# Kernel optimization log

Measured on AMD Instinct MI355X. Metric: run time of the kernel, lower is better.

The kernel has to match this reference:

```python
import jax, jax.numpy as jnp
import numpy as np

B, C, H, W = 2, 128, 64, 64
EPS = 1e-5


def setup_inputs() -> dict:
    key = jax.random.key(0)
    ks = jax.random.split(key, 8)
    sc = 1.0 / np.sqrt(C)
    inp = {
        "x": jax.random.normal(ks[0], (B, C, H, W, 2), jnp.float32),
        # naive complex BN affine params: per-channel, per-component (real/imag)
        "bn_w": jnp.ones((C, 2), jnp.float32),
        "bn_b": jnp.zeros((C, 2), jnp.float32),
        # complex 1x1 conv weights: (out_c, in_c, 2) -> [..,0]=W_real, [..,1]=W_imag
        "wq": jax.random.normal(ks[1], (C, C, 2), jnp.float32) * sc,
        "bq": jnp.zeros((C, 2), jnp.float32),
        "wk": jax.random.normal(ks[2], (C, C, 2), jnp.float32) * sc,
        "bk": jnp.zeros((C, 2), jnp.float32),
        "wv": jax.random.normal(ks[3], (C, C, 2), jnp.float32) * sc,
        "bv": jnp.zeros((C, 2), jnp.float32),
        "gamma": jnp.float32(0.05),
    }
    return inp


def _complex_bn(x, w, b):
    # naive complex BN: normalize real and imag independently per channel
    # x: (B,C,H,W,2); stats over (B,H,W) per (C, component)
    mean = x.mean(axis=(0, 2, 3), keepdims=True)
    var = x.var(axis=(0, 2, 3), keepdims=True)
    xn = (x - mean) * jax.lax.rsqrt(var + EPS)
    return xn * w[None, :, None, None, :] + b[None, :, None, None, :]


def _complex_conv1x1(x, w, b):
    # x: (B,C,H,W,2); w: (O,C,2); b: (O,2)
    xr, xi = x[..., 0], x[..., 1]
    wr, wi = w[..., 0], w[..., 1]
    yr = jnp.einsum('oc,bchw->bohw', wr, xr) - jnp.einsum('oc,bchw->bohw', wi, xi)
    yi = jnp.einsum('oc,bchw->bohw', wr, xi) + jnp.einsum('oc,bchw->bohw', wi, xr)
    yr = yr + b[:, 0][None, :, None, None]
    yi = yi + b[:, 1][None, :, None, None]
    return jnp.stack([yr, yi], axis=-1)


def _attention(x, wq, bq, wk, bk, wv, bv, gamma):
    scale = C ** (-0.5)
    N = H * W
    # q,k,v: (B,C,H,W,2) -> (B,C,N,2) -> (B,N,C,2)
    to_tokens = lambda t: t.reshape(B, C, N, 2).transpose(0, 2, 1, 3)
    q = to_tokens(_complex_conv1x1(x, wq, bq))
    k = to_tokens(_complex_conv1x1(x, wk, bk))
    v = to_tokens(_complex_conv1x1(x, wv, bv))

    qr, qi = q[..., 0], q[..., 1]          # (B,N,C)
    kr, ki = k[..., 0], -k[..., 1]         # conjugate of k
    # k_t = conj(k) with token/channel axes swapped -> (B,C,N)
    ktr = kr.transpose(0, 2, 1)
    kti = ki.transpose(0, 2, 1)

    # complex matmul q @ k_t -> only the real part is used downstream
    attn_real = jnp.einsum('bnc,bcm->bnm', qr, ktr) - jnp.einsum('bnc,bcm->bnm', qi, kti)
    attn_w = jax.nn.softmax(attn_real * scale, axis=-1)  # (B,N,N)
    # dropout = identity (eval mode)

    # attn is purely real -> complex matmul reduces to two real matmuls
    out_r = jnp.einsum('bnm,bmc->bnc', attn_w, v[..., 0])
    out_i = jnp.einsum('bnm,bmc->bnc', attn_w, v[..., 1])
    out = jnp.stack([out_r, out_i], axis=-1)              # (B,N,C,2)
    out = out.transpose(0, 2, 1, 3).reshape(B, C, H, W, 2)
    return x + gamma * out


def reference(x, bn_w, bn_b, wq, bq, wk, bk, wv, bv, gamma):
    xn = _complex_bn(x, bn_w, bn_b)
    return _attention(xn, wq, bq, wk, bk, wv, bv, gamma)
```

## Files before the change

### kernel.cpp

```cpp
#include <hip/hip_runtime.h>
#include <hip/hip_bf16.h>

typedef __bf16 bf16_t;
typedef __bf16 bf16x8 __attribute__((ext_vector_type(8)));
typedef float  f32x4  __attribute__((ext_vector_type(4)));

#define MFMA16(A,B,C) __builtin_amdgcn_mfma_f32_16x16x32_bf16((A),(B),(C),0,0,0)

constexpr int Bn = 2, Cc = 128, Hh = 64, Wd = 64;
constexpr int N  = Hh * Wd;
constexpr int T  = Bn * N;
constexpr int D  = 2 * Cc;
constexpr int NSP = 4;
constexpr float EPS = 1e-5f;
constexpr float SCL = 0.08838834764831845f * 1.4426950408889634f;

__device__ __forceinline__ int tfrag(int row, int ch) {
    return (((ch >> 5) * 4 + (row >> 4)) << 10) +
           ((((ch >> 3) & 3) * 16 + (row & 15)) << 4) + (ch & 7) * 2;
}
__device__ __forceinline__ int vfrag(int ch, int key) {
    return (((key >> 5) * 16 + (ch >> 4)) << 10) +
           ((((key >> 3) & 3) * 16 + (ch & 15)) << 4) + (key & 7) * 2;
}

__device__ __forceinline__ void gl16(const void* g, void* l) {
    __builtin_amdgcn_global_load_lds(
        (const __attribute__((address_space(1))) void*)g,
        (__attribute__((address_space(3))) void*)l, 16, 0, 0);
}

__global__ void k_pre(const float* __restrict__ x, float4* __restrict__ part,
                      const float* __restrict__ wq, const float* __restrict__ wk,
                      const float* __restrict__ wv, const float* __restrict__ bq,
                      const float* __restrict__ bk, const float* __restrict__ bv,
                      char* __restrict__ Wg, float* __restrict__ bt) {
    int tid = threadIdx.x;
    if (blockIdx.x < 512) {
        int bid = blockIdx.x;
        int q = bid >> 7, c = bid & 127;
        float sr = 0.f, si = 0.f, qr = 0.f, qi = 0.f;
        for (int b = 0; b < Bn; ++b) {
            const float2* p = (const float2*)x + (size_t)(b * Cc + c) * N + q * 1024;
            for (int i = tid; i < 1024; i += 256) {
                float2 v = p[i];
                sr += v.x; si += v.y; qr += v.x * v.x; qi += v.y * v.y;
            }
        }
        #pragma unroll
        for (int d = 32; d >= 1; d >>= 1) {
            sr += __shfl_xor(sr, d); si += __shfl_xor(si, d);
            qr += __shfl_xor(qr, d); qi += __shfl_xor(qi, d);
        }
        __shared__ float red[4][4];
        int w = tid >> 6;
        if ((tid & 63) == 0) { red[w][0] = sr; red[w][1] = si; red[w][2] = qr; red[w][3] = qi; }
        __syncthreads();
        if (tid == 0) {
            part[c * 4 + q] = make_float4(red[0][0] + red[1][0] + red[2][0] + red[3][0],
                                          red[0][1] + red[1][1] + red[2][1] + red[3][1],
                                          red[0][2] + red[1][2] + red[2][2] + red[3][2],
                                          red[0][3] + red[1][3] + red[2][3] + red[3][3]);
        }
    } else {
        int o = blockIdx.x - 512;
        int k = tid;
        int proj = o >> 8, oc = o & 255;
        const float* wsrc = proj == 0 ? wq : (proj == 1 ? wk : wv);
        const float* bsrc = proj == 0 ? bq : (proj == 1 ? bk : bv);
        int co = oc >> 7, oo = oc & 127;
        int c = k & 127, kc = k >> 7;
        float val;
        if (co == 0) val = (kc == 0) ? wsrc[(oo * 128 + c) * 2 + 0] : -wsrc[(oo * 128 + c) * 2 + 1];
        else         val = (kc == 0) ? wsrc[(oo * 128 + c) * 2 + 1] :  wsrc[(oo * 128 + c) * 2 + 0];
        int tile = o >> 6, row = o & 63;
        *(bf16_t*)(Wg + (size_t)tile * 32768 + tfrag(row, k)) = (bf16_t)val;
        if (k == 0) bt[o] = bsrc[oo * 2 + co];
    }
}

__global__ void k_norm(const float* __restrict__ x, const float4* __restrict__ part,
                       const float* __restrict__ bn_w, const float* __restrict__ bn_b,
                       char* __restrict__ XNg) {
    __shared__ float4 ssl[128];
    __shared__ __align__(16) char Tsh[32768];
    int blk = blockIdx.x;
    int b = blk >> 6, hw0 = (blk & 63) * 64;
    int tid = threadIdx.x;
    if (tid < 128) {
        float4 p0 = part[tid * 4 + 0], p1 = part[tid * 4 + 1];
        float4 p2 = part[tid * 4 + 2], p3 = part[tid * 4 + 3];
        float sr = p0.x + p1.x + p2.x + p3.x, si = p0.y + p1.y + p2.y + p3.y;
        float qr = p0.z + p1.z + p2.z + p3.z, qi = p0.w + p1.w + p2.w + p3.w;
        const float inv = 1.0f / (float)(Bn * N);
        float mr = sr * inv, mi = si * inv;
        float vr = qr * inv - mr * mr, vi = qi * inv - mi * mi;
        float scr = bn_w[tid * 2 + 0] * rsqrtf(vr + EPS);
        float sci = bn_w[tid * 2 + 1] * rsqrtf(vi + EPS);
        ssl[tid] = make_float4(scr, bn_b[tid * 2 + 0] - mr * scr,
                               sci, bn_b[tid * 2 + 1] - mi * sci);
    }
    __syncthreads();
    const float2* xin = (const float2*)x;
    #pragma unroll
    for (int it = 0; it < 32; ++it) {
        int idx = it * 256 + tid;
        int c = idx >> 6, hw = idx & 63;
        size_t gi = (size_t)(b * Cc + c) * N + hw0 + hw;
        float2 v = xin[gi];
        float4 s = ssl[c];
        *(bf16_t*)(Tsh + tfrag(hw, c))       = (bf16_t)(v.x * s.x + s.y);
        *(bf16_t*)(Tsh + tfrag(hw, c + 128)) = (bf16_t)(v.y * s.z + s.w);
    }
    __syncthreads();
    #pragma unroll
    for (int it = 0; it < 8; ++it) {
        int idx = it * 256 + tid;
        *(uint4*)(XNg + (size_t)blk * 32768 + idx * 16) = *(const uint4*)(Tsh + idx * 16);
    }
}

__global__ __launch_bounds__(256) void k_qkv(const char* __restrict__ XNg,
        const char* __restrict__ Wg, const float* __restrict__ bt,
        char* __restrict__ Qg, char* __restrict__ Kg, char* __restrict__ Vg) {
    __shared__ __align__(16) char Xsh[32768];
    __shared__ __align__(16) char Wsh[32768];
    int mx = blockIdx.x, ny = blockIdx.y;
    int tid = threadIdx.x;
    int w = tid >> 6, lane = tid & 63, n15 = lane & 15, quad = lane >> 4;
    const char* xs = XNg + (size_t)mx * 32768;
    const char* wsp = Wg + (size_t)ny * 32768;
    #pragma unroll
    for (int i = 0; i < 8; ++i) {
        int off = (w * 8 + i) * 1024 + lane * 16;
        gl16(xs + off, Xsh + off);
        gl16(wsp + off, Wsh + off);
    }
    __syncthreads();
    f32x4 acc[4] = {};
    #pragma unroll
    for (int ks = 0; ks < 8; ++ks) {
        bf16x8 a = *(const bf16x8*)(Xsh + (ks * 4 + w) * 1024 + lane * 16);
        #pragma unroll
        for (int t = 0; t < 4; ++t) {
            bf16x8 bw = *(const bf16x8*)(Wsh + (ks * 4 + t) * 1024 + lane * 16);
            acc[t] = MFMA16(a, bw, acc[t]);
        }
    }
    int proj = ny >> 2;
    int jb = (ny & 3) * 64;
    #pragma unroll
    for (int t = 0; t < 4; ++t) {
        int j = jb + t * 16 + n15;
        float bias = bt[ny * 64 + t * 16 + n15];
        #pragma unroll
        for (int r = 0; r < 4; ++r) {
            int tk = mx * 64 + w * 16 + quad * 4 + r;
            float v = acc[t][r] + bias;
            int bb = tk >> 12, n = tk & (N - 1);
            if (proj == 0) {
                *(bf16_t*)(Qg + (size_t)(tk >> 6) * 32768 + tfrag(tk & 63, j)) = (bf16_t)v;
            } else {
                size_t tb = (size_t)(bb * 64 + (n >> 6)) * 32768;
                if (proj == 1) *(bf16_t*)(Kg + tb + tfrag(n & 63, j)) = (bf16_t)v;
                else           *(bf16_t*)(Vg + tb + vfrag(j, n & 63)) = (bf16_t)v;
            }
        }
    }
}

__global__ __launch_bounds__(256, 2) void k_attn(const char* __restrict__ Qg,
        const char* __restrict__ Kg, const char* __restrict__ Vg,
        bf16_t* __restrict__ Opb, float* __restrict__ Lp) {
    __shared__ __align__(16) char Ksh[2 * 16384];
    __shared__ __align__(16) char Vsh[16384];
    __shared__ __align__(16) char Psh[4096];
    int bid = blockIdx.x;
    int grp = bid & 7, qt = bid >> 3;
    int sp = grp & 3, b = grp >> 2;
    int tid = threadIdx.x;
    int w = tid >> 6, lane = tid & 63, n15 = lane & 15, quad = lane >> 4;
    int r = w >> 1, h = w & 1;

    bf16x8 onef;
    #pragma unroll
    for (int i = 0; i < 8; ++i) onef[i] = (bf16_t)1.0f;

    bf16x8 qf[2][8];
    const char* qb = Qg + (size_t)(b * 64 + qt) * 32768;
    #pragma unroll
    for (int g = 0; g < 2; ++g)
        #pragma unroll
        for (int ks = 0; ks < 8; ++ks)
            qf[g][ks] = *(const bf16x8*)(qb + (ks * 4 + r * 2 + g) * 1024 + lane * 16);

    {
        size_t kt0 = (size_t)(b * 64 + sp * 16) * 32768;
        #pragma unroll
        for (int i = 0; i < 4; ++i) {
            int lf = w * 4 + i;
            gl16(Kg + kt0 + (((lf >> 1) * 4 + (lf & 1)) << 10) + lane * 16,
                 Ksh + (lf << 10) + lane * 16);
        }
    }

    f32x4 o[2][8] = {};
    f32x4 l_[2] = {};

    #pragma unroll 2
    for (int kt = 0; kt < 32; ++kt) {
        int cur = kt & 1;
        __syncthreads();

        size_t vt = (size_t)(b * 64 + sp * 16 + (kt >> 1)) * 32768 +
                    (size_t)(kt & 1) * 16384;
        #pragma unroll
        for (int i = 0; i < 4; ++i) {
            int off = (w * 4 + i) * 1024 + lane * 16;
            gl16(Vg + vt + off, Vsh + off);
        }
        if (kt < 31) {
            int ck = kt + 1;
            size_t ktile = (size_t)(b * 64 + sp * 16 + (ck >> 1)) * 32768;
            char* kb = Ksh + (cur ^ 1) * 16384;
            #pragma unroll
            for (int i = 0; i < 4; ++i) {
                int lf = w * 4 + i;
                gl16(Kg + ktile + (((lf >> 1) * 4 + (ck & 1) * 2 + (lf & 1)) << 10) + lane * 16,
                     kb + (lf << 10) + lane * 16);
            }
        }

        const char* kc = Ksh + cur * 16384;
        f32x4 s0 = {}, s1 = {};
        #pragma unroll
        for (int ks = 0; ks < 8; ++ks) {
            bf16x8 kf = *(const bf16x8*)(kc + ((ks * 2 + h) << 10) + lane * 16);
            s0 = MFMA16(qf[0][ks], kf, s0);
            s1 = MFMA16(qf[1][ks], kf, s1);
        }
        #pragma unroll
        for (int ri = 0; ri < 4; ++ri) {
            float p0 = __builtin_amdgcn_exp2f(s0[ri] * SCL);
            float p1 = __builtin_amdgcn_exp2f(s1[ri] * SCL);
            int base = ((h * 2 + (n15 >> 3)) * 16 + quad * 4 + ri) * 16 + (n15 & 7) * 2;
            *(bf16_t*)(Psh + ((r * 2 + 0) << 10) + base) = (bf16_t)p0;
            *(bf16_t*)(Psh + ((r * 2 + 1) << 10) + base) = (bf16_t)p1;
        }
        if (kt < 31) asm volatile("s_waitcnt vmcnt(4) lgkmcnt(0)" ::: "memory");
        else         asm volatile("s_waitcnt vmcnt(0) lgkmcnt(0)" ::: "memory");
        __builtin_amdgcn_s_barrier();
        __builtin_amdgcn_sched_barrier(0);

        bf16x8 pa0 = *(const bf16x8*)(Psh + ((r * 2 + 0) << 10) + lane * 16);
        bf16x8 pa1 = *(const bf16x8*)(Psh + ((r * 2 + 1) << 10) + lane * 16);
        l_[0] = MFMA16(pa0, onef, l_[0]);
        l_[1] = MFMA16(pa1, onef, l_[1]);
        #pragma unroll
        for (int ct = 0; ct < 8; ++ct) {
            bf16x8 vf = *(const bf16x8*)(Vsh + ((h * 8 + ct) << 10) + lane * 16);
            o[0][ct] = MFMA16(pa0, vf, o[0][ct]);
            o[1][ct] = MFMA16(pa1, vf, o[1][ct]);
        }
    }
    int tok0 = b * N + qt * 64 + r * 32;
    #pragma unroll
    for (int g = 0; g < 2; ++g) {
        #pragma unroll
        for (int ct = 0; ct < 8; ++ct)
            #pragma unroll
            for (int ri = 0; ri < 4; ++ri)
                Opb[((size_t)sp * T + tok0 + g * 16 + quad * 4 + ri) * D +
                    h * 128 + ct * 16 + n15] = (bf16_t)o[g][ct][ri];
        if (h == 0 && n15 == 0) {
            #pragma unroll
            for (int ri = 0; ri < 4; ++ri)
                Lp[sp * T + tok0 + g * 16 + quad * 4 + ri] = l_[g][ri];
        }
    }
}

__global__ void k_comb(const bf16_t* __restrict__ Opb, const float* __restrict__ Lp,
                       const float4* __restrict__ part, const float* __restrict__ bn_w,
                       const float* __restrict__ bn_b, const float* __restrict__ x,
                       const float* __restrict__ gamma, float* __restrict__ out) {
    __shared__ float4 ssl[128];
    __shared__ float wts[32];
    __shared__ float Ot[256 * 33];
    int blk = blockIdx.x;
    int b = blk >> 7, hw0 = (blk & 127) * 32;
    int tok0 = b * N + hw0;
    int tid = threadIdx.x;
    if (tid < 128) {
        float4 p0 = part[tid * 4 + 0], p1 = part[tid * 4 + 1];
        float4 p2 = part[tid * 4 + 2], p3 = part[tid * 4 + 3];
        float sr = p0.x + p1.x + p2.x + p3.x, si = p0.y + p1.y + p2.y + p3.y;
        float qr = p0.z + p1.z + p2.z + p3.z, qi = p0.w + p1.w + p2.w + p3.w;
        const float inv = 1.0f / (float)(Bn * N);
        float mr = sr * inv, mi = si * inv;
        float vr = qr * inv - mr * mr, vi = qi * inv - mi * mi;
        float scr = bn_w[tid * 2 + 0] * rsqrtf(vr + EPS);
        float sci = bn_w[tid * 2 + 1] * rsqrtf(vi + EPS);
        ssl[tid] = make_float4(scr, bn_b[tid * 2 + 0] - mr * scr,
                               sci, bn_b[tid * 2 + 1] - mi * sci);
    }
    if (tid < 32) {
        float Z = 0.f;
        #pragma unroll
        for (int s = 0; s < NSP; ++s) Z += Lp[s * T + tok0 + tid];
        wts[tid] = gamma[0] / Z;
    }
    __syncthreads();
    #pragma unroll
    for (int i = 0; i < 4; ++i) {
        int idx = i * 256 + tid;
        int tk = idx >> 5, chunk = idx & 31;
        size_t base = (size_t)(tok0 + tk) * D + chunk * 8;
        float acc[8] = {};
        #pragma unroll
        for (int s = 0; s < NSP; ++s) {
            bf16x8 v = *(const bf16x8*)(Opb + (size_t)s * T * D + base);
            #pragma unroll
            for (int j = 0; j < 8; ++j) acc[j] += (float)v[j];
        }
        float ww = wts[tk];
        #pragma unroll
        for (int j = 0; j < 8; ++j) Ot[(chunk * 8 + j) * 33 + tk] = acc[j] * ww;
    }
    __syncthreads();
    const float2* xin = (const float2*)x;
    float2* xo = (float2*)out;
    #pragma unroll
    for (int i = 0; i < 16; ++i) {
        int linear = i * 256 + tid;
        int c = linear >> 5, hwo = linear & 31;
        size_t idx = (size_t)(b * Cc + c) * N + hw0 + hwo;
        float2 v = xin[idx];
        float4 s = ssl[c];
        float2 res;
        res.x = v.x * s.x + s.y + Ot[c * 33 + hwo];
        res.y = v.y * s.z + s.w + Ot[(128 + c) * 33 + hwo];
        xo[idx] = res;
    }
}

extern "C" void kernel_launch(void* const* d_in, const int* in_sizes, int n_in,
                              void* d_out, int out_size, void* d_ws, size_t ws_size,
                              hipStream_t stream) {
    const float* x    = (const float*)d_in[0];
    const float* bn_w = (const float*)d_in[1];
    const float* bn_b = (const float*)d_in[2];
    const float* wq   = (const float*)d_in[3];
    const float* bq   = (const float*)d_in[4];
    const float* wk   = (const float*)d_in[5];
    const float* bk   = (const float*)d_in[6];
    const float* wv   = (const float*)d_in[7];
    const float* bv   = (const float*)d_in[8];
    const float* gam  = (const float*)d_in[9];
    float* out = (float*)d_out;

    char* ws = (char*)d_ws;
    size_t off = 0;
    auto alloc = [&](size_t bytes) -> void* {
        void* p = ws + off;
        off += (bytes + 255) & ~(size_t)255;
        return p;
    };
    float4* part = (float4*)alloc(512 * sizeof(float4));
    char*   XNg  = (char*)alloc((size_t)128 * 32768);
    char*   Wg   = (char*)alloc((size_t)12 * 32768);
    float*  bt   = (float*)alloc(768 * 4);
    char*   Qg   = (char*)alloc((size_t)128 * 32768);
    char*   Kg   = (char*)alloc((size_t)128 * 32768);
    char*   Vg   = (char*)alloc((size_t)128 * 32768);
    bf16_t* Opb  = (bf16_t*)alloc((size_t)NSP * T * D * 2);
    float*  Lp   = (float*)alloc((size_t)NSP * T * 4);

    k_pre<<<1280, 256, 0, stream>>>(x, part, wq, wk, wv, bq, bk, bv, Wg, bt);
    k_norm<<<128, 256, 0, stream>>>(x, part, bn_w, bn_b, XNg);
    k_qkv<<<dim3(128, 12), 256, 0, stream>>>(XNg, Wg, bt, Qg, Kg, Vg);
    k_attn<<<512, 256, 0, stream>>>(Qg, Kg, Vg, Opb, Lp);
    k_comb<<<256, 256, 0, stream>>>(Opb, Lp, part, bn_w, bn_b, x, gam, out);
}
```

Baseline: 153.4 us.

## Double attention key splits and feed V fragments from global into registers

The key dimension is split 8 ways instead of 4, so 1024 attention blocks are launched instead of 512. Each wave now owns 64 output columns for all 64 query rows and loads its V fragments straight from global memory into registers, which removes the V staging buffer in LDS and its barrier wait. MFMA sections are bracketed with s_setprio, and the launch-bounds occupancy hint is dropped. The trade-off is twice as much partial-output and row-sum traffic for the combine kernel to read and reduce, plus each loop iteration now waits on all outstanding global loads (vmcnt(0)).

```diff
diff --git a/kernel.cpp b/kernel.cpp
--- a/kernel.cpp
+++ b/kernel.cpp
@@ -11,7 +11,7 @@
 constexpr int N  = Hh * Wd;
 constexpr int T  = Bn * N;
 constexpr int D  = 2 * Cc;
-constexpr int NSP = 4;
+constexpr int NSP = 8;
 constexpr float EPS = 1e-5f;
 constexpr float SCL = 0.08838834764831845f * 1.4426950408889634f;
 
@@ -169,15 +169,14 @@
     }
 }
 
-__global__ __launch_bounds__(256, 2) void k_attn(const char* __restrict__ Qg,
+__global__ __launch_bounds__(256) void k_attn(const char* __restrict__ Qg,
         const char* __restrict__ Kg, const char* __restrict__ Vg,
         bf16_t* __restrict__ Opb, float* __restrict__ Lp) {
     __shared__ __align__(16) char Ksh[2 * 16384];
-    __shared__ __align__(16) char Vsh[16384];
     __shared__ __align__(16) char Psh[4096];
     int bid = blockIdx.x;
-    int grp = bid & 7, qt = bid >> 3;
-    int sp = grp & 3, b = grp >> 2;
+    int grp = bid & 15, qt = bid >> 4;
+    int sp = grp & 7, b = grp >> 3;
     int tid = threadIdx.x;
     int w = tid >> 6, lane = tid & 63, n15 = lane & 15, quad = lane >> 4;
     int r = w >> 1, h = w & 1;
@@ -194,51 +193,53 @@
         for (int ks = 0; ks < 8; ++ks)
             qf[g][ks] = *(const bf16x8*)(qb + (ks * 4 + r * 2 + g) * 1024 + lane * 16);
 
-    {
-        size_t kt0 = (size_t)(b * 64 + sp * 16) * 32768;
-        #pragma unroll
-        for (int i = 0; i < 4; ++i) {
-            int lf = w * 4 + i;
-            gl16(Kg + kt0 + (((lf >> 1) * 4 + (lf & 1)) << 10) + lane * 16,
-                 Ksh + (lf << 10) + lane * 16);
-        }
-    }
-
-    f32x4 o[2][8] = {};
-    f32x4 l_[2] = {};
-
-    #pragma unroll 2
-    for (int kt = 0; kt < 32; ++kt) {
+    size_t kbase = (size_t)(b * 64 + sp * 8) * 32768;
+    #pragma unroll
+    for (int i = 0; i < 4; ++i) {
+        int lf = w * 4 + i;
+        gl16(Kg + kbase + (((lf >> 1) * 4 + (lf & 1)) << 10) + lane * 16,
+             Ksh + (lf << 10) + lane * 16);
+    }
+
+    f32x4 o[4][4] = {};
+    f32x4 l_[4] = {};
+
+    for (int kt = 0; kt < 16; ++kt) {
         int cur = kt & 1;
-        __syncthreads();
-
-        size_t vt = (size_t)(b * 64 + sp * 16 + (kt >> 1)) * 32768 +
-                    (size_t)(kt & 1) * 16384;
-        #pragma unroll
-        for (int i = 0; i < 4; ++i) {
-            int off = (w * 4 + i) * 1024 + lane * 16;
-            gl16(Vg + vt + off, Vsh + off);
-        }
-        if (kt < 31) {
+        asm volatile("s_waitcnt vmcnt(0)" ::: "memory");
+        __builtin_amdgcn_s_barrier();
+        __builtin_amdgcn_sched_barrier(0);
+
+        bf16x8 vf[4];
+        const char* vt = Vg + kbase + (size_t)(kt >> 1) * 32768 + (kt & 1) * 16384;
+        #pragma unroll
+        for (int ct = 0; ct < 4; ++ct)
+            vf[ct] = *(const bf16x8*)(vt + ((w * 4 + ct) << 10) + lane * 16);
+        __builtin_amdgcn_sched_barrier(0);
+
+        if (kt < 15) {
             int ck = kt + 1;
-            size_t ktile = (size_t)(b * 64 + sp * 16 + (ck >> 1)) * 32768;
             char* kb = Ksh + (cur ^ 1) * 16384;
             #pragma unroll
             for (int i = 0; i < 4; ++i) {
                 int lf = w * 4 + i;
-                gl16(Kg + ktile + (((lf >> 1) * 4 + (ck & 1) * 2 + (lf & 1)) << 10) + lane * 16,
+                gl16(Kg + kbase + (size_t)(ck >> 1) * 32768 +
+                         (((lf >> 1) * 4 + (ck & 1) * 2 + (lf & 1)) << 10) + lane * 16,
                      kb + (lf << 10) + lane * 16);
             }
         }
 
         const char* kc = Ksh + cur * 16384;
         f32x4 s0 = {}, s1 = {};
+        __builtin_amdgcn_s_setprio(1);
         #pragma unroll
         for (int ks = 0; ks < 8; ++ks) {
             bf16x8 kf = *(const bf16x8*)(kc + ((ks * 2 + h) << 10) + lane * 16);
             s0 = MFMA16(qf[0][ks], kf, s0);
             s1 = MFMA16(qf[1][ks], kf, s1);
         }
+        __builtin_amdgcn_s_setprio(0);
+
         #pragma unroll
         for (int ri = 0; ri < 4; ++ri) {
             float p0 = __builtin_amdgcn_exp2f(s0[ri] * SCL);
@@ -247,36 +248,42 @@
             *(bf16_t*)(Psh + ((r * 2 + 0) << 10) + base) = (bf16_t)p0;
             *(bf16_t*)(Psh + ((r * 2 + 1) << 10) + base) = (bf16_t)p1;
         }
-        if (kt < 31) asm volatile("s_waitcnt vmcnt(4) lgkmcnt(0)" ::: "memory");
-        else         asm volatile("s_waitcnt vmcnt(0) lgkmcnt(0)" ::: "memory");
+        asm volatile("s_waitcnt lgkmcnt(0)" ::: "memory");
         __builtin_amdgcn_s_barrier();
         __builtin_amdgcn_sched_barrier(0);
 
-        bf16x8 pa0 = *(const bf16x8*)(Psh + ((r * 2 + 0) << 10) + lane * 16);
-        bf16x8 pa1 = *(const bf16x8*)(Psh + ((r * 2 + 1) << 10) + lane * 16);
-        l_[0] = MFMA16(pa0, onef, l_[0]);
-        l_[1] = MFMA16(pa1, onef, l_[1]);
-        #pragma unroll
-        for (int ct = 0; ct < 8; ++ct) {
-            bf16x8 vf = *(const bf16x8*)(Vsh + ((h * 8 + ct) << 10) + lane * 16);
-            o[0][ct] = MFMA16(pa0, vf, o[0][ct]);
-            o[1][ct] = MFMA16(pa1, vf, o[1][ct]);
-        }
-    }
-    int tok0 = b * N + qt * 64 + r * 32;
-    #pragma unroll
-    for (int g = 0; g < 2; ++g) {
-        #pragma unroll
-        for (int ct = 0; ct < 8; ++ct)
+        bf16x8 pa[4];
+        #pragma unroll
+        for (int rf = 0; rf < 4; ++rf)
+            pa[rf] = *(const bf16x8*)(Psh + (rf << 10) + lane * 16);
+        __builtin_amdgcn_s_setprio(1);
+        if (w == 0) {
+            #pragma unroll
+            for (int rf = 0; rf < 4; ++rf)
+                l_[rf] = MFMA16(pa[rf], onef, l_[rf]);
+        }
+        #pragma unroll
+        for (int rf = 0; rf < 4; ++rf)
+            #pragma unroll
+            for (int ct = 0; ct < 4; ++ct)
+                o[rf][ct] = MFMA16(pa[rf], vf[ct], o[rf][ct]);
+        __builtin_amdgcn_s_setprio(0);
+    }
+    int tok0 = b * N + qt * 64;
+    #pragma unroll
+    for (int rf = 0; rf < 4; ++rf)
+        #pragma unroll
+        for (int ct = 0; ct < 4; ++ct)
             #pragma unroll
             for (int ri = 0; ri < 4; ++ri)
-                Opb[((size_t)sp * T + tok0 + g * 16 + quad * 4 + ri) * D +
-                    h * 128 + ct * 16 + n15] = (bf16_t)o[g][ct][ri];
-        if (h == 0 && n15 == 0) {
+                Opb[((size_t)sp * T + tok0 + rf * 16 + quad * 4 + ri) * D +
+                    w * 64 + ct * 16 + n15] = (bf16_t)o[rf][ct][ri];
+    if (w == 0 && n15 == 0) {
+        #pragma unroll
+        for (int rf = 0; rf < 4; ++rf)
             #pragma unroll
             for (int ri = 0; ri < 4; ++ri)
-                Lp[sp * T + tok0 + g * 16 + quad * 4 + ri] = l_[g][ri];
-        }
+                Lp[sp * T + tok0 + rf * 16 + quad * 4 + ri] = l_[rf][ri];
     }
 }
 
@@ -379,6 +386,6 @@
     k_pre<<<1280, 256, 0, stream>>>(x, part, wq, wk, wv, bq, bk, bv, Wg, bt);
     k_norm<<<128, 256, 0, stream>>>(x, part, bn_w, bn_b, XNg);
     k_qkv<<<dim3(128, 12), 256, 0, stream>>>(XNg, Wg, bt, Qg, Kg, Vg);
-    k_attn<<<512, 256, 0, stream>>>(Qg, Kg, Vg, Opb, Lp);
+    k_attn<<<1024, 256, 0, stream>>>(Qg, Kg, Vg, Opb, Lp);
     k_comb<<<256, 256, 0, stream>>>(Opb, Lp, part, bn_w, bn_b, x, gam, out);
 }
```

After: 160.1 us. +4.3%, slower.
